# Performance work log

Measured on AMD Instinct MI355X. Metric: run time of the kernel, lower is better.

Reference implementation:

```python
import jax, jax.numpy as jnp
import numpy as np
from jax import lax

_F1 = np.array([1., 3., 3., 1.], dtype=np.float32)
_F1 = _F1 / _F1.sum()
F2D = jnp.asarray(np.outer(_F1, _F1))  # [4,4] normalized FIR filter
LRELU_GAIN = float(np.sqrt(2.0))


def _upfirdn2d_up(x, up, pad0, pad1, gain):
    # zero-insertion upsample + pad + FIR filter (VALID depthwise conv)
    B, C, H, W = x.shape
    if up > 1:
        x = jnp.zeros((B, C, H, up, W, up), x.dtype).at[:, :, :, 0, :, 0].set(x)
        x = x.reshape(B, C, H * up, W * up)
    x = jnp.pad(x, ((0, 0), (0, 0), (pad0, pad1), (pad0, pad1)))
    k = jnp.broadcast_to((F2D * gain).astype(x.dtype), (C, 1, 4, 4))
    return lax.conv_general_dilated(x, k, (1, 1), 'VALID', feature_group_count=C)


def _affine(w, aw, ab):
    # FullyConnectedLayer: weight_gain = 1/sqrt(in_features), bias_init handled in setup
    return w @ aw.T * (1.0 / np.sqrt(aw.shape[1])) + ab


def _mod_conv(x, weight, styles, up):
    # fused modulated conv2d with demodulation, batch-as-groups trick
    B = x.shape[0]
    O, I, kh, kw = weight.shape
    w = weight[None] * styles[:, None, :, None, None]          # [B,O,I,kh,kw]
    d = lax.rsqrt(jnp.sum(jnp.square(w), axis=(2, 3, 4)) + 1e-8)  # [B,O]
    w = w * d[:, :, None, None, None]
    if up == 2:
        # conv2d_resample: FIR upsample (gain=up^2), then true conv (flipped weight)
        # padding=1, fw=4, up=2 -> px0 = 1 + (4+2-1)//2 = 3, px1 = 1 + (4-2)//2 = 2
        x = _upfirdn2d_up(x, 2, 3, 2, 4.0)
        w = w[:, :, :, ::-1, ::-1]
        pad = 'VALID'
    else:
        pad = ((kh // 2, kh // 2), (kw // 2, kw // 2))
    xr = x.reshape(1, B * I, x.shape[2], x.shape[3])
    wr = w.reshape(B * O, I, kh, kw)
    y = lax.conv_general_dilated(xr, wr, (1, 1), pad, feature_group_count=B)
    return y.reshape(B, O, y.shape[2], y.shape[3])


def _lrelu_bias(x, b, clamp=256.0):
    # bias_act: lrelu(x+b) * sqrt(2), clamp
    x = x + b[None, :, None, None]
    x = jnp.where(x >= 0, x, 0.2 * x) * LRELU_GAIN
    return jnp.clip(x, -clamp, clamp)


def setup_inputs() -> dict:
    key = jax.random.key(0)
    ks = jax.random.split(key, 12)
    B, Cin, Cout, Wd, R, IC = 8, 512, 512, 512, 64, 3
    r = R // 2
    return dict(
        x=jax.random.normal(ks[0], (B, Cin, r, r), jnp.float32),
        img=jax.random.normal(ks[1], (B, IC, r, r), jnp.float32),
        ws=jax.random.normal(ks[2], (B, 3, Wd), jnp.float32),
        a0_w=jax.random.normal(ks[3], (Cin, Wd), jnp.float32),
        a0_b=jnp.ones((Cin,), jnp.float32),
        w0=jax.random.normal(ks[4], (Cout, Cin, 3, 3), jnp.float32),
        b0=jnp.zeros((Cout,), jnp.float32),
        ns0=jnp.asarray(0.1, jnp.float32),
        nc0=jax.random.normal(ks[5], (R, R), jnp.float32),
        a1_w=jax.random.normal(ks[6], (Cout, Wd), jnp.float32),
        a1_b=jnp.ones((Cout,), jnp.float32),
        w1=jax.random.normal(ks[7], (Cout, Cout, 3, 3), jnp.float32),
        b1=jnp.zeros((Cout,), jnp.float32),
        ns1=jnp.asarray(0.1, jnp.float32),
        nc1=jax.random.normal(ks[8], (R, R), jnp.float32),
        at_w=jax.random.normal(ks[9], (Cout, Wd), jnp.float32),
        at_b=jnp.ones((Cout,), jnp.float32),
        wt=jax.random.normal(ks[10], (IC, Cout), jnp.float32),
        bt=jnp.zeros((IC,), jnp.float32),
    )


def reference(x, img, ws, a0_w, a0_b, w0, b0, ns0, nc0,
              a1_w, a1_b, w1, b1, ns1, nc1, at_w, at_b, wt, bt):
    # conv0: modulated conv, up=2, const noise, lrelu bias-act with clamp
    s0 = _affine(ws[:, 0], a0_w, a0_b)
    h = _mod_conv(x, w0, s0, up=2)
    h = h + nc0[None, None] * ns0
    h = _lrelu_bias(h, b0)
    # conv1: modulated conv, up=1
    s1 = _affine(ws[:, 1], a1_w, a1_b)
    h = _mod_conv(h, w1, s1, up=1)
    h = h + nc1[None, None] * ns1
    h = _lrelu_bias(h, b1)
    # skip architecture: upsample img (upsample2d: px0=2, px1=1, gain=4)
    img_up = _upfirdn2d_up(img, 2, 2, 1, 4.0)
    # torgb: 1x1 modulated conv, no demodulation, styles scaled by weight_gain
    st = _affine(ws[:, 2], at_w, at_b) * (1.0 / np.sqrt(wt.shape[1]))
    y = jnp.einsum('bihw,bi,oi->bohw', h, st, wt)
    y = jnp.clip(y + bt[None, :, None, None], -256.0, 256.0)
    return h, img_up + y
```

## Files before the change

### kernel.cpp

```cpp
#include <hip/hip_runtime.h>
#include <stdint.h>

typedef unsigned short u16;
typedef unsigned int   u32;

#define DEVINL __device__ __forceinline__

typedef __bf16 bf16x8 __attribute__((ext_vector_type(8)));
typedef float  f32x4  __attribute__((ext_vector_type(4)));

#define RSQRT512 0.044194173824159216f
#define LRELU_G  1.4142135623730951f

DEVINL u16 f2bf(float f) {
  union { float f; u32 u; } v; v.f = f;
  u32 r = v.u + 0x7fffu + ((v.u >> 16) & 1u);
  return (u16)(r >> 16);
}
DEVINL float bf2f(u16 b) {
  union { u32 u; float f; } v; v.u = ((u32)b) << 16;
  return v.f;
}

#define AS1 __attribute__((address_space(1)))
#define AS3 __attribute__((address_space(3)))
DEVINL void gload16(const void* g, void* l) {
  __builtin_amdgcn_global_load_lds((AS1 const u32*)(uintptr_t)g,
                                   (AS3 u32*)(u32)(uintptr_t)l, 16, 0, 0);
}

__global__ __launch_bounds__(256)
void style_kernel(const float* __restrict__ wsin,
                  const float* __restrict__ a0w, const float* __restrict__ a0b,
                  const float* __restrict__ a1w, const float* __restrict__ a1b,
                  const float* __restrict__ atw, const float* __restrict__ atb,
                  float* __restrict__ s_all)
{
  int wid = threadIdx.x >> 6, lane = threadIdx.x & 63;
  int idx = blockIdx.x * 4 + wid;
  int j = idx >> 12;
  int b = (idx >> 9) & 7;
  int o = idx & 511;
  const float* A  = (j == 0) ? a0w : ((j == 1) ? a1w : atw);
  const float* Ab = (j == 0) ? a0b : ((j == 1) ? a1b : atb);
  const float* wv = wsin + (b * 3 + j) * 512;
  float p = 0.f;
  #pragma unroll
  for (int m = 0; m < 512; m += 64) p += wv[m + lane] * A[(size_t)o * 512 + m + lane];
  #pragma unroll
  for (int s = 32; s; s >>= 1) p += __shfl_xor(p, s, 64);
  if (lane == 0) {
    float v = p * RSQRT512 + Ab[o];
    if (j == 2) v *= RSQRT512;
    s_all[idx] = v;
  }
}

template <int FLIP>
__global__ __launch_bounds__(256)
void wprep_kernel(const float* __restrict__ w, const float* __restrict__ s_j,
                  u16* __restrict__ wg)
{
  int b = blockIdx.x >> 9;
  int o = blockIdx.x & 511;
  __shared__ float s_sh[512];
  __shared__ float red[4];
  int t = threadIdx.x;
  s_sh[t]       = s_j[b * 512 + t];
  s_sh[t + 256] = s_j[b * 512 + t + 256];
  __syncthreads();
  float wv[2][9];
  float ssq = 0.f;
  #pragma unroll
  for (int hh = 0; hh < 2; ++hh) {
    int i = t + hh * 256;
    float si = s_sh[i];
    const float* wp = w + ((size_t)o * 512 + i) * 9;
    #pragma unroll
    for (int k = 0; k < 9; ++k) { float v = wp[k] * si; wv[hh][k] = v; ssq += v * v; }
  }
  #pragma unroll
  for (int s = 32; s; s >>= 1) ssq += __shfl_xor(ssq, s, 64);
  if ((t & 63) == 0) red[t >> 6] = ssq;
  __syncthreads();
  float d = red[0] + red[1] + red[2] + red[3];
  d = 1.0f / sqrtf(d + 1e-8f);
  u16* outb = wg + (size_t)b * 2359296;
  #pragma unroll
  for (int hh = 0; hh < 2; ++hh) {
    int i = t + hh * 256;
    int kq = i >> 3, e = i & 7;
    #pragma unroll
    for (int ky = 0; ky < 3; ++ky)
      #pragma unroll
      for (int kx = 0; kx < 3; ++kx) {
        int tap = FLIP ? ((2 - ky) * 3 + (2 - kx)) : (ky * 3 + kx);
        outb[(((size_t)(tap * 64 + kq)) * 512 + o) * 8 + e] = f2bf(wv[hh][ky * 3 + kx] * d);
      }
  }
}

__global__ __launch_bounds__(256)
void transpose_x(const float* __restrict__ x, float* __restrict__ xt)
{
  int b = blockIdx.x >> 5, y = blockIdx.x & 31;
  __shared__ __align__(16) float lds[32][260];
  int t = threadIdx.x;
  #pragma unroll 1
  for (int half = 0; half < 2; ++half) {
    for (int idx = t; idx < 8192; idx += 256) {
      int xq = idx & 31, i = idx >> 5;
      lds[xq][i] = x[(((size_t)(b * 512 + half * 256 + i)) << 10) + (y << 5) + xq];
    }
    __syncthreads();
    for (int idx = t; idx < 2048; idx += 256) {
      int xq = idx >> 6, i4 = idx & 63;
      float4 v = *(const float4*)&lds[xq][i4 * 4];
      *(float4*)&xt[((size_t)((b * 32 + y) * 32 + xq) << 9) + half * 256 + i4 * 4] = v;
    }
    __syncthreads();
  }
}

__global__ __launch_bounds__(256)
void upblur_kernel(const float* __restrict__ xt, u16* __restrict__ xb)
{
  int b = blockIdx.x / 66, p = blockIdx.x - b * 66;
  int t = threadIdx.x;
  int ch = t << 1;
  int c8 = ch >> 3, e = ch & 7;
  int m0, m1; float wy0, wy1;
  if ((p & 1) == 0) { m0 = (p >> 1) - 1; wy0 = 0.75f; m1 = p >> 1;       wy1 = 0.25f; }
  else              { m0 = (p - 3) >> 1; wy0 = 0.25f; m1 = (p - 1) >> 1; wy1 = 0.75f; }
  bool vm0 = (unsigned)m0 < 32u, vm1 = (unsigned)m1 < 32u;
  const float* base = xt + (size_t)b * 524288;
  u16* ob = xb + (((size_t)(b * 64 + c8) * 66 + p) * 66) * 8 + e;
  for (int q = 0; q < 66; ++q) {
    int n0, n1; float wx0, wx1;
    if ((q & 1) == 0) { n0 = (q >> 1) - 1; wx0 = 0.75f; n1 = q >> 1;       wx1 = 0.25f; }
    else              { n0 = (q - 3) >> 1; wx0 = 0.25f; n1 = (q - 1) >> 1; wx1 = 0.75f; }
    bool vn0 = (unsigned)n0 < 32u, vn1 = (unsigned)n1 < 32u;
    float a0 = 0.f, a1 = 0.f;
    if (vm0 & vn0) { float2 u = *(const float2*)(base + (((size_t)m0 * 32 + n0) << 9) + ch);
                     float w = wy0 * wx0; a0 += w * u.x; a1 += w * u.y; }
    if (vm0 & vn1) { float2 u = *(const float2*)(base + (((size_t)m0 * 32 + n1) << 9) + ch);
                     float w = wy0 * wx1; a0 += w * u.x; a1 += w * u.y; }
    if (vm1 & vn0) { float2 u = *(const float2*)(base + (((size_t)m1 * 32 + n0) << 9) + ch);
                     float w = wy1 * wx0; a0 += w * u.x; a1 += w * u.y; }
    if (vm1 & vn1) { float2 u = *(const float2*)(base + (((size_t)m1 * 32 + n1) << 9) + ch);
                     float w = wy1 * wx1; a0 += w * u.x; a1 += w * u.y; }
    u32 outv = (u32)f2bf(a0) | ((u32)f2bf(a1) << 16);
    *(u32*)(ob + (size_t)q * 8) = outv;
  }
}

extern __shared__ u16 dynLds[];

template <int EPI>
__global__ __launch_bounds__(512, 2)
void conv8(const u16* __restrict__ xin,
           const u16* __restrict__ wg,
           const float* __restrict__ noise,
           const float* __restrict__ nsp,
           const float* __restrict__ bias,
           u16* __restrict__ hpOut,
           float* __restrict__ hOut)
{
  int blk = (blockIdx.x & 7) * 32 + (blockIdx.x >> 3);
  int b  = blk >> 5;
  int ot = (blk >> 4) & 1;
  int pt = blk & 15;
  int o0 = ot << 8;
  int y0 = pt << 2;

  int t = threadIdx.x;
  int w = t >> 6;
  int lane = t & 63;
  int gq = lane >> 4, r = lane & 15;
  int wm = w >> 2;
  int wn = w & 3;

  u16* Wb0 = dynLds;
  u16* Wb1 = dynLds + 16384;
  u16* Xb0 = dynLds + 32768;
  u16* Xb1 = dynLds + 49152;

  f32x4 acc[8][4];
  #pragma unroll
  for (int i = 0; i < 8; ++i)
    #pragma unroll
    for (int j = 0; j < 4; ++j) acc[i][j] = (f32x4){0.f, 0.f, 0.f, 0.f};

  const u16* wbB = wg + (size_t)b * 2359296;
  const u16* xbB = xin + (size_t)b * 2230272;

  auto STAGE = [&](int tile, int pb) {
    int tap = tile >> 3;
    int ck  = tile & 7;
    int dy = (tap * 171) >> 9;
    int dx = tap - dy * 3;
    u16* dW = (pb ? Wb1 : Wb0) + w * 2048;
    u16* dX = (pb ? Xb1 : Xb0) + w * 2048;
    const u16* wsrc = wbB + ((size_t)(tap * 64 + ck * 8 + w)) * 4096 + (size_t)o0 * 8;
    const u16* xsrc = xbB + ((size_t)(ck * 8 + w) * 66) * 66 * 8;
    #pragma unroll
    for (int q = 0; q < 4; ++q) {
      int row = q * 64 + lane;
      gload16(wsrc + (size_t)row * 8, dW + q * 512);
      int yy = y0 + q + dy;
      int xx = lane + dx;
      gload16(xsrc + (((size_t)yy * 66) + xx) * 8, dX + q * 512);
    }
  };

  auto TILE = [&](int pb) {
    const u16* Wp = pb ? Wb1 : Wb0;
    const u16* Xp = pb ? Xb1 : Xb0;
    const u16* A = (EPI == 0) ? Xp : Wp;
    const u16* B = (EPI == 0) ? Wp : Xp;
    bf16x8 bfr[4][2];
    #pragma unroll
    for (int fb = 0; fb < 4; ++fb)
      #pragma unroll
      for (int kk = 0; kk < 2; ++kk)
        bfr[fb][kk] = *(const bf16x8*)&B[((kk * 4 + gq) << 11) + ((wn * 64 + fb * 16 + r) << 3)];
    __builtin_amdgcn_s_setprio(1);
    #pragma unroll
    for (int fa = 0; fa < 8; ++fa) {
      int rowA = (wm * 128 + fa * 16 + r) << 3;
      bf16x8 a0 = *(const bf16x8*)&A[(gq << 11) + rowA];
      bf16x8 a1 = *(const bf16x8*)&A[((4 + gq) << 11) + rowA];
      #pragma unroll
      for (int fb = 0; fb < 4; ++fb) {
        acc[fa][fb] = __builtin_amdgcn_mfma_f32_16x16x32_bf16(a0, bfr[fb][0], acc[fa][fb], 0, 0, 0);
        acc[fa][fb] = __builtin_amdgcn_mfma_f32_16x16x32_bf16(a1, bfr[fb][1], acc[fa][fb], 0, 0, 0);
      }
    }
    __builtin_amdgcn_s_setprio(0);
  };

  STAGE(0, 0);
  STAGE(1, 1);
  asm volatile("s_waitcnt vmcnt(8)" ::: "memory");
  __builtin_amdgcn_sched_barrier(0);
  __builtin_amdgcn_s_barrier();
  __builtin_amdgcn_sched_barrier(0);

  int p = 0;
  #pragma unroll 1
  for (int tl = 0; tl < 72; ++tl) {
    TILE(p);
    __builtin_amdgcn_sched_barrier(0);
    __builtin_amdgcn_s_barrier();
    __builtin_amdgcn_sched_barrier(0);
    if (tl < 70) {
      STAGE(tl + 2, p);
      asm volatile("s_waitcnt vmcnt(8)" ::: "memory");
    } else if (tl == 70) {
      asm volatile("s_waitcnt vmcnt(0)" ::: "memory");
    }
    __builtin_amdgcn_sched_barrier(0);
    __builtin_amdgcn_s_barrier();
    __builtin_amdgcn_sched_barrier(0);
    p ^= 1;
  }
  __builtin_amdgcn_sched_barrier(0);

  float ns = nsp[0];
  if constexpr (EPI == 0) {
    #pragma unroll
    for (int fa = 0; fa < 8; ++fa) {
      #pragma unroll
      for (int fb = 0; fb < 4; ++fb) {
        int oo = o0 + wn * 64 + fb * 16 + r;
        float bo = bias[oo];
        #pragma unroll
        for (int v = 0; v < 4; ++v) {
          int px = wm * 128 + fa * 16 + gq * 4 + v;
          int pg = (pt << 8) + px;
          int y = pg >> 6, x2 = pg & 63;
          float val = acc[fa][fb][v] + noise[pg] * ns + bo;
          val = (val >= 0.f ? val : 0.2f * val) * LRELU_G;
          val = fminf(fmaxf(val, -256.f), 256.f);
          hpOut[((((size_t)b * 64 + (oo >> 3)) * 66 + (y + 1)) * 66 + (x2 + 1)) * 8 + (oo & 7)] = f2bf(val);
        }
      }
    }
  } else {
    #pragma unroll
    for (int fa = 0; fa < 8; ++fa) {
      #pragma unroll
      for (int fb = 0; fb < 4; ++fb) {
        int px = wn * 64 + fb * 16 + r;
        int pg = (pt << 8) + px;
        float nv = noise[pg] * ns;
        #pragma unroll
        for (int v = 0; v < 4; ++v) {
          int oo = o0 + wm * 128 + fa * 16 + gq * 4 + v;
          float val = acc[fa][fb][v] + nv + bias[oo];
          val = (val >= 0.f ? val : 0.2f * val) * LRELU_G;
          val = fminf(fmaxf(val, -256.f), 256.f);
          hOut[((size_t)(b * 512 + oo) << 12) + pg] = val;
        }
      }
    }
  }
}

__global__ __launch_bounds__(256)
void torgb_kernel(const float* __restrict__ h, const float* __restrict__ s_all,
                  const float* __restrict__ wt, const float* __restrict__ bt,
                  const float* __restrict__ img, float* __restrict__ out2)
{
  int b = blockIdx.x >> 4;
  int y = ((blockIdx.x & 15) << 2) + (threadIdx.x >> 6);
  int x = threadIdx.x & 63;
  __shared__ float stw[3][512];
  const float* st = s_all + 2 * 4096 + b * 512;
  for (int i = threadIdx.x; i < 512; i += 256) {
    float s = st[i];
    stw[0][i] = s * wt[i];
    stw[1][i] = s * wt[512 + i];
    stw[2][i] = s * wt[1024 + i];
  }
  __syncthreads();
  const float* hp = h + ((size_t)b * 512 << 12) + (y << 6) + x;
  float a0 = 0.f, a1 = 0.f, a2 = 0.f;
  #pragma unroll 8
  for (int i = 0; i < 512; ++i) {
    float v = hp[(size_t)i << 12];
    a0 += v * stw[0][i]; a1 += v * stw[1][i]; a2 += v * stw[2][i];
  }
  float accs[3] = {a0, a1, a2};
  int my0, my1; float wy0, wy1;
  if ((y & 1) == 0) { my0 = (y >> 1) - 1; wy0 = 0.25f; my1 = y >> 1;       wy1 = 0.75f; }
  else              { my0 = y >> 1;       wy0 = 0.75f; my1 = (y >> 1) + 1; wy1 = 0.25f; }
  int mx0, mx1; float wx0, wx1;
  if ((x & 1) == 0) { mx0 = (x >> 1) - 1; wx0 = 0.25f; mx1 = x >> 1;       wx1 = 0.75f; }
  else              { mx0 = x >> 1;       wx0 = 0.75f; mx1 = (x >> 1) + 1; wx1 = 0.25f; }
  bool vy0 = (unsigned)my0 < 32u, vy1 = (unsigned)my1 < 32u;
  bool vx0 = (unsigned)mx0 < 32u, vx1 = (unsigned)mx1 < 32u;
  #pragma unroll
  for (int o = 0; o < 3; ++o) {
    float yv = fminf(fmaxf(accs[o] + bt[o], -256.f), 256.f);
    const float* ib = img + ((size_t)(b * 3 + o) << 10);
    float iu = 0.f;
    if (vy0 & vx0) iu += wy0 * wx0 * ib[(my0 << 5) + mx0];
    if (vy0 & vx1) iu += wy0 * wx1 * ib[(my0 << 5) + mx1];
    if (vy1 & vx0) iu += wy1 * wx0 * ib[(my1 << 5) + mx0];
    if (vy1 & vx1) iu += wy1 * wx1 * ib[(my1 << 5) + mx1];
    out2[((size_t)(b * 3 + o) << 12) + (y << 6) + x] = iu + yv;
  }
}

extern "C" void kernel_launch(void* const* d_in, const int* in_sizes, int n_in,
                              void* d_out, int out_size, void* d_ws, size_t ws_size,
                              hipStream_t stream) {
  (void)in_sizes; (void)n_in; (void)out_size; (void)ws_size;
  const float* x   = (const float*)d_in[0];
  const float* img = (const float*)d_in[1];
  const float* ws_ = (const float*)d_in[2];
  const float* a0w = (const float*)d_in[3];
  const float* a0b = (const float*)d_in[4];
  const float* w0  = (const float*)d_in[5];
  const float* b0  = (const float*)d_in[6];
  const float* ns0 = (const float*)d_in[7];
  const float* nc0 = (const float*)d_in[8];
  const float* a1w = (const float*)d_in[9];
  const float* a1b = (const float*)d_in[10];
  const float* w1  = (const float*)d_in[11];
  const float* b1  = (const float*)d_in[12];
  const float* ns1 = (const float*)d_in[13];
  const float* nc1 = (const float*)d_in[14];
  const float* atw = (const float*)d_in[15];
  const float* atb = (const float*)d_in[16];
  const float* wt  = (const float*)d_in[17];
  const float* bt  = (const float*)d_in[18];

  char* wsp = (char*)d_ws;
  float* s_all = (float*)wsp;
  u16* wg0 = (u16*)(wsp + 49152);
  u16* wg1 = (u16*)(wsp + 49152 + 37748736ull);
  u16* xb  = (u16*)(wsp + 49152 + 2ull * 37748736);
  u16* hp  = (u16*)(wsp + 49152 + 2ull * 37748736 + 35684352);
  float* xtf = (float*)hp;

  float* h_out = (float*)d_out;
  float* out2  = (float*)d_out + 16777216;

  hipFuncSetAttribute((const void*)conv8<0>,
                      hipFuncAttributeMaxDynamicSharedMemorySize, 131072);
  hipFuncSetAttribute((const void*)conv8<1>,
                      hipFuncAttributeMaxDynamicSharedMemorySize, 131072);

  style_kernel<<<3072, 256, 0, stream>>>(ws_, a0w, a0b, a1w, a1b, atw, atb, s_all);
  wprep_kernel<1><<<4096, 256, 0, stream>>>(w0, s_all, wg0);
  wprep_kernel<0><<<4096, 256, 0, stream>>>(w1, s_all + 4096, wg1);
  transpose_x<<<256, 256, 0, stream>>>(x, xtf);
  upblur_kernel<<<528, 256, 0, stream>>>(xtf, xb);
  hipMemsetAsync(hp, 0, 35684352, stream);
  conv8<0><<<256, 512, 131072, stream>>>(xb, wg0, nc0, ns0, b0, hp, nullptr);
  conv8<1><<<256, 512, 131072, stream>>>(hp, wg1, nc1, ns1, b1, nullptr, h_out);
  torgb_kernel<<<128, 256, 0, stream>>>(h_out, s_all, wt, bt, img, out2);
}
```

Before: 471.5 us.

## Split weight prep into demod and vectorized pack kernels; restructure upblur

Weight modulation is split into a demodulation-norm kernel and a pack kernel that writes 8 bf16 values per 16-byte store, replacing scattered 2-byte stores. The upsample-blur kernel is reorganised so each block handles one 8-channel group for a batch, iterating rows. This aims to coalesce the large packed-weight writes, at the cost of reading the weights twice and using strided reads in the pack kernel.

```diff
diff --git a/kernel.cpp b/kernel.cpp
--- a/kernel.cpp
+++ b/kernel.cpp
@@ -8,6 +8,7 @@
 
 typedef __bf16 bf16x8 __attribute__((ext_vector_type(8)));
 typedef float  f32x4  __attribute__((ext_vector_type(4)));
+typedef unsigned short u16x8 __attribute__((ext_vector_type(8)));
 
 #define RSQRT512 0.044194173824159216f
 #define LRELU_G  1.4142135623730951f
@@ -56,10 +57,9 @@
   }
 }
 
-template <int FLIP>
-__global__ __launch_bounds__(256)
-void wprep_kernel(const float* __restrict__ w, const float* __restrict__ s_j,
-                  u16* __restrict__ wg)
+__global__ __launch_bounds__(256)
+void demod_kernel(const float* __restrict__ w, const float* __restrict__ s_j,
+                  float* __restrict__ dOut)
 {
   int b = blockIdx.x >> 9;
   int o = blockIdx.x & 511;
@@ -69,7 +69,6 @@
   s_sh[t]       = s_j[b * 512 + t];
   s_sh[t + 256] = s_j[b * 512 + t + 256];
   __syncthreads();
-  float wv[2][9];
   float ssq = 0.f;
   #pragma unroll
   for (int hh = 0; hh < 2; ++hh) {
@@ -77,26 +76,45 @@
     float si = s_sh[i];
     const float* wp = w + ((size_t)o * 512 + i) * 9;
     #pragma unroll
-    for (int k = 0; k < 9; ++k) { float v = wp[k] * si; wv[hh][k] = v; ssq += v * v; }
+    for (int k = 0; k < 9; ++k) { float v = wp[k] * si; ssq += v * v; }
   }
   #pragma unroll
   for (int s = 32; s; s >>= 1) ssq += __shfl_xor(ssq, s, 64);
   if ((t & 63) == 0) red[t >> 6] = ssq;
   __syncthreads();
-  float d = red[0] + red[1] + red[2] + red[3];
-  d = 1.0f / sqrtf(d + 1e-8f);
-  u16* outb = wg + (size_t)b * 2359296;
-  #pragma unroll
-  for (int hh = 0; hh < 2; ++hh) {
-    int i = t + hh * 256;
-    int kq = i >> 3, e = i & 7;
-    #pragma unroll
-    for (int ky = 0; ky < 3; ++ky)
+  if (t == 0) {
+    float d = red[0] + red[1] + red[2] + red[3];
+    dOut[b * 512 + o] = 1.0f / sqrtf(d + 1e-8f);
+  }
+}
+
+template <int FLIP>
+__global__ __launch_bounds__(256)
+void wpack_kernel(const float* __restrict__ w, const float* __restrict__ s_j,
+                  const float* __restrict__ dIn, u16* __restrict__ wg)
+{
+  int b = blockIdx.x >> 6;
+  int kq = blockIdx.x & 63;
+  float sv[8];
+  #pragma unroll
+  for (int e = 0; e < 8; ++e) sv[e] = s_j[b * 512 + kq * 8 + e];
+  int t = threadIdx.x;
+  #pragma unroll 1
+  for (int rep = 0; rep < 2; ++rep) {
+    int o = rep * 256 + t;
+    float d = dIn[b * 512 + o];
+    const float* wp = w + ((size_t)o * 512 + kq * 8) * 9;
+    float wv[72];
+    #pragma unroll
+    for (int j = 0; j < 72; ++j) wv[j] = wp[j];
+    #pragma unroll
+    for (int tapOut = 0; tapOut < 9; ++tapOut) {
+      int ksrc = FLIP ? (8 - tapOut) : tapOut;
+      u16x8 g;
       #pragma unroll
-      for (int kx = 0; kx < 3; ++kx) {
-        int tap = FLIP ? ((2 - ky) * 3 + (2 - kx)) : (ky * 3 + kx);
-        outb[(((size_t)(tap * 64 + kq)) * 512 + o) * 8 + e] = f2bf(wv[hh][ky * 3 + kx] * d);
-      }
+      for (int e = 0; e < 8; ++e) g[e] = f2bf(wv[e * 9 + ksrc] * sv[e] * d);
+      *(u16x8*)&wg[((((size_t)(b * 9 + tapOut)) * 64 + kq) * 512 + o) * 8] = g;
+    }
   }
 }
 
@@ -125,32 +143,30 @@
 __global__ __launch_bounds__(256)
 void upblur_kernel(const float* __restrict__ xt, u16* __restrict__ xb)
 {
-  int b = blockIdx.x / 66, p = blockIdx.x - b * 66;
+  int b = blockIdx.x >> 6, c8 = blockIdx.x & 63;
+  const float* base = xt + (size_t)b * 524288 + c8 * 8;
+  u16* ob = xb + ((size_t)(b * 64 + c8)) * 34848;
   int t = threadIdx.x;
-  int ch = t << 1;
-  int c8 = ch >> 3, e = ch & 7;
-  int m0, m1; float wy0, wy1;
-  if ((p & 1) == 0) { m0 = (p >> 1) - 1; wy0 = 0.75f; m1 = p >> 1;       wy1 = 0.25f; }
-  else              { m0 = (p - 3) >> 1; wy0 = 0.25f; m1 = (p - 1) >> 1; wy1 = 0.75f; }
-  bool vm0 = (unsigned)m0 < 32u, vm1 = (unsigned)m1 < 32u;
-  const float* base = xt + (size_t)b * 524288;
-  u16* ob = xb + (((size_t)(b * 64 + c8) * 66 + p) * 66) * 8 + e;
-  for (int q = 0; q < 66; ++q) {
-    int n0, n1; float wx0, wx1;
-    if ((q & 1) == 0) { n0 = (q >> 1) - 1; wx0 = 0.75f; n1 = q >> 1;       wx1 = 0.25f; }
-    else              { n0 = (q - 3) >> 1; wx0 = 0.25f; n1 = (q - 1) >> 1; wx1 = 0.75f; }
-    bool vn0 = (unsigned)n0 < 32u, vn1 = (unsigned)n1 < 32u;
-    float a0 = 0.f, a1 = 0.f;
-    if (vm0 & vn0) { float2 u = *(const float2*)(base + (((size_t)m0 * 32 + n0) << 9) + ch);
-                     float w = wy0 * wx0; a0 += w * u.x; a1 += w * u.y; }
-    if (vm0 & vn1) { float2 u = *(const float2*)(base + (((size_t)m0 * 32 + n1) << 9) + ch);
-                     float w = wy0 * wx1; a0 += w * u.x; a1 += w * u.y; }
-    if (vm1 & vn0) { float2 u = *(const float2*)(base + (((size_t)m1 * 32 + n0) << 9) + ch);
-                     float w = wy1 * wx0; a0 += w * u.x; a1 += w * u.y; }
-    if (vm1 & vn1) { float2 u = *(const float2*)(base + (((size_t)m1 * 32 + n1) << 9) + ch);
-                     float w = wy1 * wx1; a0 += w * u.x; a1 += w * u.y; }
-    u32 outv = (u32)f2bf(a0) | ((u32)f2bf(a1) << 16);
-    *(u32*)(ob + (size_t)q * 8) = outv;
+  #pragma unroll 1
+  for (int p = 0; p < 66; ++p) {
+    int m0, m1; float wy0, wy1;
+    if ((p & 1) == 0) { m0 = (p >> 1) - 1; wy0 = 0.75f; m1 = p >> 1;       wy1 = 0.25f; }
+    else              { m0 = (p - 3) >> 1; wy0 = 0.25f; m1 = (p - 1) >> 1; wy1 = 0.75f; }
+    bool vm0 = (unsigned)m0 < 32u, vm1 = (unsigned)m1 < 32u;
+    #pragma unroll 1
+    for (int idx = t; idx < 528; idx += 256) {
+      int x = idx >> 3, e = idx & 7;
+      int n0, n1; float wx0, wx1;
+      if ((x & 1) == 0) { n0 = (x >> 1) - 1; wx0 = 0.75f; n1 = x >> 1;       wx1 = 0.25f; }
+      else              { n0 = (x - 3) >> 1; wx0 = 0.25f; n1 = (x - 1) >> 1; wx1 = 0.75f; }
+      bool vn0 = (unsigned)n0 < 32u, vn1 = (unsigned)n1 < 32u;
+      float a = 0.f;
+      if (vm0 & vn0) a += wy0 * wx0 * base[((m0 * 32 + n0) << 9) + e];
+      if (vm0 & vn1) a += wy0 * wx1 * base[((m0 * 32 + n1) << 9) + e];
+      if (vm1 & vn0) a += wy1 * wx0 * base[((m1 * 32 + n0) << 9) + e];
+      if (vm1 & vn1) a += wy1 * wx1 * base[((m1 * 32 + n1) << 9) + e];
+      ob[(p * 66 + x) * 8 + e] = f2bf(a);
+    }
   }
 }
 
@@ -383,6 +399,8 @@
   u16* wg1 = (u16*)(wsp + 49152 + 37748736ull);
   u16* xb  = (u16*)(wsp + 49152 + 2ull * 37748736);
   u16* hp  = (u16*)(wsp + 49152 + 2ull * 37748736 + 35684352);
+  float* d0 = (float*)(wsp + 49152 + 2ull * 37748736 + 2ull * 35684352);
+  float* d1 = (float*)(wsp + 49152 + 2ull * 37748736 + 2ull * 35684352 + 16384);
   float* xtf = (float*)hp;
 
   float* h_out = (float*)d_out;
@@ -394,10 +412,12 @@
                       hipFuncAttributeMaxDynamicSharedMemorySize, 131072);
 
   style_kernel<<<3072, 256, 0, stream>>>(ws_, a0w, a0b, a1w, a1b, atw, atb, s_all);
-  wprep_kernel<1><<<4096, 256, 0, stream>>>(w0, s_all, wg0);
-  wprep_kernel<0><<<4096, 256, 0, stream>>>(w1, s_all + 4096, wg1);
+  demod_kernel<<<4096, 256, 0, stream>>>(w0, s_all, d0);
+  demod_kernel<<<4096, 256, 0, stream>>>(w1, s_all + 4096, d1);
+  wpack_kernel<1><<<512, 256, 0, stream>>>(w0, s_all, d0, wg0);
+  wpack_kernel<0><<<512, 256, 0, stream>>>(w1, s_all + 4096, d1, wg1);
   transpose_x<<<256, 256, 0, stream>>>(x, xtf);
-  upblur_kernel<<<528, 256, 0, stream>>>(xtf, xb);
+  upblur_kernel<<<512, 256, 0, stream>>>(xtf, xb);
   hipMemsetAsync(hp, 0, 35684352, stream);
   conv8<0><<<256, 512, 131072, stream>>>(xb, wg0, nc0, ns0, b0, hp, nullptr);
   conv8<1><<<256, 512, 131072, stream>>>(hp, wg1, nc1, ns1, b1, nullptr, h_out);
```

Result: slower. 536.8 us (+13.8%).
